# Performance work log

Measured on AMD Instinct MI355X. Metric: run time of the kernel, lower is better.

Reference implementation:

```python
import jax, jax.numpy as jnp
import numpy as np

B, L, C, S, W, R = 2, 16, 64, 64, 128, 32
MOD_HIDDEN = 32


def _conv3d(x, k, b, pad_hw):
    # x: (B,C,L,S,W), k: (O,I,1,kh,kw)
    y = jax.lax.conv_general_dilated(
        x, k, window_strides=(1, 1, 1),
        padding=((0, 0), (pad_hw, pad_hw), (pad_hw, pad_hw)),
        dimension_numbers=('NCDHW', 'OIDHW', 'NCDHW'))
    return y + b[None, :, None, None, None]


def setup_inputs() -> dict:
    key = jax.random.key(0)
    ks = jax.random.split(key, 16)
    d = {}
    d['x'] = jax.random.normal(ks[0], (B, L, C, S, W), jnp.float32)
    u1 = jax.random.uniform(ks[1], (C, R), jnp.float32)
    u2 = jax.random.uniform(ks[2], (C, R), jnp.float32)
    r_min, r_max = 0.8, 0.99
    d['nu_log'] = jnp.log(-0.5 * jnp.log(u1 * (r_max ** 2 - r_min ** 2) + r_min ** 2))
    d['theta_log'] = jnp.log(u2 * jnp.float32(2 * np.pi))
    d['disp_nu'] = jnp.zeros((C, R), jnp.float32)
    d['disp_theta'] = jnp.zeros((C, R), jnp.float32)
    d['mlp_w1'] = jax.random.normal(ks[3], (C, MOD_HIDDEN), jnp.float32) / np.sqrt(C).astype(np.float32)
    d['mlp_b1'] = jnp.zeros((MOD_HIDDEN,), jnp.float32)
    d['mlp_w2'] = jax.random.normal(ks[4], (MOD_HIDDEN, C * R * 2), jnp.float32) / np.sqrt(MOD_HIDDEN).astype(np.float32)
    d['mlp_b2'] = jnp.zeros((C * R * 2,), jnp.float32)
    d['forcing_scale'] = jnp.float32(0.1)
    d['U_row_r'] = jax.random.normal(ks[5], (C, S, R), jnp.float32) / np.sqrt(S).astype(np.float32)
    d['U_row_i'] = jax.random.normal(ks[6], (C, S, R), jnp.float32) / np.sqrt(S).astype(np.float32)
    d['V_col_r'] = jax.random.normal(ks[7], (C, W, R), jnp.float32) / np.sqrt(W).astype(np.float32)
    d['V_col_i'] = jax.random.normal(ks[8], (C, W, R), jnp.float32) / np.sqrt(W).astype(np.float32)
    d['proj_W_r'] = jax.random.normal(ks[9], (C, C), jnp.float32) / np.sqrt(C).astype(np.float32)
    d['proj_W_i'] = jax.random.normal(ks[10], (C, C), jnp.float32) / np.sqrt(C).astype(np.float32)
    d['proj_b_r'] = jnp.zeros((C,), jnp.float32)
    d['proj_b_i'] = jnp.zeros((C,), jnp.float32)
    fan = np.sqrt(C * 9).astype(np.float32)
    d['convr_k'] = jax.random.normal(ks[11], (C, C, 1, 3, 3), jnp.float32) / fan
    d['convr_b'] = jnp.zeros((C,), jnp.float32)
    d['convi_k'] = jax.random.normal(ks[12], (C, C, 1, 3, 3), jnp.float32) / fan
    d['convi_b'] = jnp.zeros((C,), jnp.float32)
    d['fuse_k'] = jax.random.normal(ks[13], (C, 2 * C, 1, 1, 1), jnp.float32) / np.sqrt(2 * C).astype(np.float32)
    d['fuse_b'] = jnp.zeros((C,), jnp.float32)
    d['ln_g'] = jnp.ones((S, W), jnp.float32)
    d['ln_b'] = jnp.zeros((S, W), jnp.float32)
    return d


def reference(x, nu_log, theta_log, disp_nu, disp_theta, mlp_w1, mlp_b1,
              mlp_w2, mlp_b2, forcing_scale, U_row_r, U_row_i, V_col_r,
              V_col_i, proj_W_r, proj_W_i, proj_b_r, proj_b_i, convr_k,
              convr_b, convi_k, convi_b, fuse_k, fuse_b, ln_g, ln_b):
    # Diagonal LRU poles lam = exp(-exp(nu) + i*exp(theta)), per (C,R)
    nu = jnp.exp(nu_log + disp_nu)
    theta = jnp.exp(theta_log + disp_theta)
    lam = jnp.exp(jax.lax.complex(-nu, theta))
    gamma = jnp.sqrt(jnp.clip(1.0 - jnp.abs(lam) ** 2, 1e-6, None))

    # Selective input-dependent forcing from spatially-pooled context
    ctx = x.mean(axis=(-2, -1))  # (B,L,C)
    f = jnp.tanh(ctx @ mlp_w1 + mlp_b1) @ mlp_w2 + mlp_b2
    f = f.reshape(ctx.shape[0], ctx.shape[1], C, R, 2)
    forcing = forcing_scale * jax.lax.complex(f[..., 0], f[..., 1])  # (B,L,C,R)

    # Low-rank complex spatial projection to rank-R state per channel
    U = jax.lax.complex(U_row_r, U_row_i)  # (C,S,R)
    V = jax.lax.complex(V_col_r, V_col_i)  # (C,W,R)
    xc = x.astype(jnp.complex64)
    u = jnp.einsum('blcsw,csr->blcwr', xc, jnp.conj(U))
    u = jnp.einsum('blcwr,cwr->blcr', u, jnp.conj(V))  # (B,L,C,R)
    u = gamma * u * (1.0 + forcing)

    # Diagonal linear recurrence h_t = lam*h_{t-1} + u_t via associative scan over L
    A = jnp.broadcast_to(lam[None, None], u.shape)

    def comb(e1, e2):
        a1, b1 = e1
        a2, b2 = e2
        return a1 * a2, a2 * b1 + b2

    _, h = jax.lax.associative_scan(comb, (A, u), axis=1)

    # Reconstruct spatial field from low-rank states
    t = jnp.einsum('blcr,csr->blcsr', h, U)
    y = jnp.einsum('blcsr,cwr->blcsw', t, V)  # (B,L,C,S,W) complex

    projW = jax.lax.complex(proj_W_r, proj_W_i)
    projb = jax.lax.complex(proj_b_r, proj_b_i)
    y = jnp.einsum('blcsw,oc->blosw', y, projW) + projb[None, None, :, None, None]

    # Post-recurrence spatial convs on real/imag parts, fuse, layernorm, residual
    yr = jnp.transpose(jnp.real(y), (0, 2, 1, 3, 4))  # (B,C,L,S,W)
    yi = jnp.transpose(jnp.imag(y), (0, 2, 1, 3, 4))
    yr = _conv3d(yr, convr_k, convr_b, 1)
    yi = _conv3d(yi, convi_k, convi_b, 1)
    fused = _conv3d(jnp.concatenate([yr, yi], axis=1), fuse_k, fuse_b, 0)
    fused = jnp.transpose(fused, (0, 2, 1, 3, 4))  # (B,L,C,S,W)

    mu = fused.mean(axis=(-2, -1), keepdims=True)
    var = fused.var(axis=(-2, -1), keepdims=True)
    normed = (fused - mu) / jnp.sqrt(var + 1e-5) * ln_g + ln_b
    return normed + x
```

## Files before the change

kernel.cpp:

```cpp
#include <hip/hip_runtime.h>

typedef unsigned short u16;
typedef unsigned int u32;
typedef __attribute__((ext_vector_type(8))) short short8;
typedef __attribute__((ext_vector_type(4))) float f32x4;

constexpr int B = 2, L = 16, C = 64, S = 64, W = 128, R = 32, MH = 32;
constexpr int BL = B * L;
constexpr int SW = S * W;
constexpr int CR = C * R;
constexpr int F2 = C * R * 2;

__device__ __forceinline__ float us2f(u16 h) { return __uint_as_float(((u32)h) << 16); }
__device__ __forceinline__ float bf_lo(u32 u) { return __uint_as_float(u << 16); }
__device__ __forceinline__ float bf_hi(u32 u) { return __uint_as_float(u & 0xffff0000u); }
__device__ __forceinline__ u16 f2bu(float f) {
  u32 u = __float_as_uint(f);
  u32 r = (u + 0x7fffu + ((u >> 16) & 1u)) >> 16;
  return (u16)r;
}
__device__ __forceinline__ u32 pack2(float lo, float hi) {
  return (u32)f2bu(lo) | ((u32)f2bu(hi) << 16);
}

__global__ void k_prep(const float* __restrict__ nu_log, const float* __restrict__ th_log,
                       const float* __restrict__ dnu, const float* __restrict__ dth,
                       float* __restrict__ lamr, float* __restrict__ lami,
                       float* __restrict__ gam) {
  int i = blockIdx.x * 256 + threadIdx.x;
  if (i >= CR) return;
  float nu = expf(nu_log[i] + dnu[i]);
  float th = expf(th_log[i] + dth[i]);
  float mag = expf(-nu);
  lamr[i] = mag * cosf(th);
  lami[i] = mag * sinf(th);
  gam[i] = sqrtf(fmaxf(1.0f - mag * mag, 1e-6f));
}

__global__ void k_keff(const float* __restrict__ fuse_k, const float* __restrict__ fuse_b,
                       const float* __restrict__ convr_k, const float* __restrict__ convr_b,
                       const float* __restrict__ convi_k, const float* __restrict__ convi_b,
                       u16* __restrict__ keff_bf, float* __restrict__ biaseff) {
  int i = blockIdx.x * 256 + threadIdx.x;
  if (i < C * 2 * C * 9) {
    int o = i / (2 * C * 9);
    int rem = i - o * (2 * C * 9);
    int cin2 = rem / 9;
    int seg = rem - cin2 * 9;
    const float* ck = (cin2 < C) ? convr_k : convi_k;
    int cin = cin2 & (C - 1);
    int fbase = o * 2 * C + ((cin2 < C) ? 0 : C);
    float acc = 0.f;
    for (int m = 0; m < C; ++m)
      acc += fuse_k[fbase + m] * ck[(m * C + cin) * 9 + seg];
    int kstep = cin2 >> 5;
    int kk = cin2 & 31;
    int lane = (o & 15) | ((kk >> 3) << 4);
    int j = kk & 7;
    int m_tile = o >> 4;
    keff_bf[((((seg * 4 + kstep) * 4 + m_tile) * 64 + lane) << 3) + j] = f2bu(acc);
  } else if (i < C * 2 * C * 9 + C) {
    int o = i - C * 2 * C * 9;
    float acc = fuse_b[o];
    for (int m = 0; m < C; ++m) {
      acc += fuse_k[o * 2 * C + m] * convr_b[m];
      acc += fuse_k[o * 2 * C + C + m] * convi_b[m];
    }
    biaseff[o] = acc;
  }
}

__global__ void k_apack(const float* __restrict__ pWr, const float* __restrict__ pWi,
                        u16* __restrict__ aproj) {
  int i = blockIdx.x * 256 + threadIdx.x;
  if (i >= 128 * 128) return;
  int m = i >> 7, k = i & 127;
  int c = k >> 1, im = k & 1;
  int o = m & 63;
  float v;
  if (m < 64) v = im ? -pWi[o * 64 + c] : pWr[o * 64 + c];
  else        v = im ?  pWr[o * 64 + c] : pWi[o * 64 + c];
  aproj[i] = f2bu(v);
}

__global__ __launch_bounds__(256) void k_mlp(
    const float* __restrict__ ctx, const float* __restrict__ w1, const float* __restrict__ b1,
    const float* __restrict__ w2, const float* __restrict__ b2, const float* __restrict__ fscale,
    float* __restrict__ forcing) {
  int bl = blockIdx.x >> 4;
  int kt = blockIdx.x & 15;
  int k0 = kt * 256;
  __shared__ float cv[C];
  __shared__ float hid[MH];
  __shared__ float lw2[MH * 256];
  int t = threadIdx.x;
  if (t < C) cv[t] = ctx[bl * C + t];
  for (int i = t; i < MH * 64; i += 256) {
    int j = i >> 6, q = i & 63;
    ((float4*)lw2)[i] = ((const float4*)(w2 + (size_t)j * F2 + k0))[q];
  }
  __syncthreads();
  if (t < MH) {
    float a = b1[t];
    for (int c2 = 0; c2 < C; ++c2) a += cv[c2] * w1[c2 * MH + t];
    hid[t] = tanhf(a);
  }
  __syncthreads();
  float scale = fscale[0];
  float a = b2[k0 + t];
#pragma unroll
  for (int j = 0; j < MH; ++j) a += hid[j] * lw2[j * 256 + t];
  forcing[(size_t)bl * F2 + k0 + t] = scale * a;
}

__global__ __launch_bounds__(256) void k_enc(
    const float* __restrict__ x,
    const float* __restrict__ Vr, const float* __restrict__ Vi,
    const float* __restrict__ Ur, const float* __restrict__ Ui,
    float* __restrict__ ctx, float* __restrict__ u) {
  int blc = blockIdx.x;
  int c = blc & (C - 1);
  __shared__ __align__(16) char smem[17408 * 2 + 16384 + 64];
  u16* xt = (u16*)smem;
  u16* bt = (u16*)(smem + 17408);
  float* uldr = (float*)(smem + 34816);
  float* uldi = uldr + 2048;
  float* y1  = (float*)smem;
  float* part = (float*)(smem + 17408);
  float* red = (float*)(smem + 17408 * 2 + 16384);
  int t = threadIdx.x;
  int lane = t & 63, wv = t >> 6;
  float sm = 0.f;
  {
    const float4* xp = (const float4*)(x + (size_t)blc * SW);
    for (int i = t; i < SW / 4; i += 256) {
      float4 v = xp[i];
      sm += v.x + v.y + v.z + v.w;
      int idx = i * 4, s = idx >> 7, w = idx & 127;
      u32* d = (u32*)&xt[s * 136 + w];
      d[0] = pack2(v.x, v.y);
      d[1] = pack2(v.z, v.w);
    }
  }
#pragma unroll
  for (int o = 32; o > 0; o >>= 1) sm += __shfl_down(sm, o, 64);
  if (lane == 0) red[wv] = sm;
  {
    const float* vrp = Vr + (size_t)c * 4096;
    const float* vip = Vi + (size_t)c * 4096;
    for (int i = t; i < 4096; i += 256) {
      int w = i >> 5, r = i & 31;
      bt[r * 136 + w]        = f2bu(vrp[i]);
      bt[(32 + r) * 136 + w] = f2bu(-vip[i]);
    }
  }
  {
    const float* urp = Ur + (size_t)c * 2048;
    const float* uip = Ui + (size_t)c * 2048;
    for (int i = t; i < 2048; i += 256) { uldr[i] = urp[i]; uldi[i] = uip[i]; }
  }
  __syncthreads();
  if (t == 0) ctx[blc] = (red[0] + red[1] + red[2] + red[3]) * (1.f / SW);
  int quad = lane >> 4, l15 = lane & 15;
  f32x4 zf = {0.f, 0.f, 0.f, 0.f};
  f32x4 acc[4] = {zf, zf, zf, zf};
#pragma unroll
  for (int ks = 0; ks < 4; ++ks) {
    int kofs = ks * 32 + quad * 8;
    short8 bf = *(const short8*)&bt[(wv * 16 + l15) * 136 + kofs];
#pragma unroll
    for (int mt = 0; mt < 4; ++mt) {
      short8 af = *(const short8*)&xt[(mt * 16 + l15) * 136 + kofs];
      acc[mt] = __builtin_amdgcn_mfma_f32_16x16x32_bf16(af, bf, acc[mt], 0, 0, 0);
    }
  }
  __syncthreads();
#pragma unroll
  for (int mt = 0; mt < 4; ++mt)
#pragma unroll
    for (int reg = 0; reg < 4; ++reg)
      y1[(mt * 16 + quad * 4 + reg) * 65 + wv * 16 + l15] = acc[mt][reg];
  __syncthreads();
  {
    int r = t & 31, sg = t >> 5;
    float pr = 0.f, pi = 0.f;
#pragma unroll
    for (int k = 0; k < 8; ++k) {
      int s = sg * 8 + k;
      float yr = y1[s * 65 + r], yi = y1[s * 65 + 32 + r];
      float ur = uldr[s * 32 + r], ui = uldi[s * 32 + r];
      pr += ur * yr + ui * yi;
      pi += ur * yi - ui * yr;
    }
    part[sg * 64 + r * 2]     = pr;
    part[sg * 64 + r * 2 + 1] = pi;
  }
  __syncthreads();
  if (t < 32) {
    float pr = 0.f, pi = 0.f;
#pragma unroll
    for (int sg = 0; sg < 8; ++sg) {
      pr += part[sg * 64 + t * 2];
      pi += part[sg * 64 + t * 2 + 1];
    }
    u[((size_t)blc * R + t) * 2]     = pr;
    u[((size_t)blc * R + t) * 2 + 1] = pi;
  }
}

__global__ void k_scan(const float* __restrict__ lamr, const float* __restrict__ lami,
                       const float* __restrict__ gam, const float* __restrict__ forcing,
                       const float* __restrict__ u, float* __restrict__ h) {
  int i = blockIdx.x * 256 + threadIdx.x;
  if (i >= B * CR) return;
  int b = i / CR;
  int cr = i - b * CR;
  float lr = lamr[cr], li = lami[cr], g = gam[cr];
  float hr = 0.f, hi = 0.f;
  for (int l = 0; l < L; ++l) {
    size_t off = ((size_t)(b * L + l) * CR + cr) * 2;
    float ur0 = u[off], ui0 = u[off + 1];
    float fr = forcing[off], fi = forcing[off + 1];
    float ofr = 1.f + fr;
    float ur = g * (ur0 * ofr - ui0 * fi);
    float ui = g * (ur0 * fi + ui0 * ofr);
    float nr = lr * hr - li * hi + ur;
    float ni = lr * hi + li * hr + ui;
    hr = nr; hi = ni;
    h[off] = hr; h[off + 1] = hi;
  }
}

__global__ __launch_bounds__(256) void k_decode(
    const float* __restrict__ h,
    const float* __restrict__ Ur, const float* __restrict__ Ui,
    const float* __restrict__ Vr, const float* __restrict__ Vi,
    u32* __restrict__ y_cm32, int bl_base) {
  int bid = blockIdx.x;
  int c = bid & 63;
  int blh = bid >> 6;
  int bl = bl_base + blh;
  __shared__ __align__(16) u16 ldA[64 * 72];
  __shared__ __align__(16) u16 ldBr[128 * 72];
  __shared__ __align__(16) u16 ldBi[128 * 72];
  int t = threadIdx.x;
  {
    const float* hp = h + ((size_t)(bl * C + c) * R) * 2;
    const float* urp = Ur + (size_t)c * (S * R);
    const float* uip = Ui + (size_t)c * (S * R);
    for (int p = t; p < S * R; p += 256) {
      int s = p >> 5, r = p & 31;
      float hr = hp[r * 2], hi = hp[r * 2 + 1];
      float ur = urp[p], ui = uip[p];
      ldA[s * 72 + r]      = f2bu(hr * ur - hi * ui);
      ldA[s * 72 + 32 + r] = f2bu(hr * ui + hi * ur);
    }
  }
  {
    const float* vrp = Vr + (size_t)c * (W * R);
    const float* vip = Vi + (size_t)c * (W * R);
    for (int p = t; p < W * R; p += 256) {
      int w = p >> 5, r = p & 31;
      float vr = vrp[p], vi = vip[p];
      ldBr[w * 72 + r]      = f2bu(vr);
      ldBr[w * 72 + 32 + r] = f2bu(-vi);
      ldBi[w * 72 + r]      = f2bu(vi);
      ldBi[w * 72 + 32 + r] = f2bu(vr);
    }
  }
  __syncthreads();
  int lane = t & 63, q = t >> 6;
  int quad = lane >> 4, l15 = lane & 15;
  f32x4 zf = {0.f, 0.f, 0.f, 0.f};
  f32x4 accr[4][2], acci[4][2];
#pragma unroll
  for (int mt = 0; mt < 4; ++mt)
#pragma unroll
    for (int nt = 0; nt < 2; ++nt) { accr[mt][nt] = zf; acci[mt][nt] = zf; }
#pragma unroll
  for (int ks = 0; ks < 2; ++ks) {
    int kofs = ks * 32 + quad * 8;
    short8 af[4];
#pragma unroll
    for (int mt = 0; mt < 4; ++mt)
      af[mt] = *(const short8*)&ldA[(mt * 16 + l15) * 72 + kofs];
#pragma unroll
    for (int nt = 0; nt < 2; ++nt) {
      int wrow = q * 32 + nt * 16 + l15;
      short8 br = *(const short8*)&ldBr[wrow * 72 + kofs];
      short8 bi = *(const short8*)&ldBi[wrow * 72 + kofs];
#pragma unroll
      for (int mt = 0; mt < 4; ++mt) {
        accr[mt][nt] = __builtin_amdgcn_mfma_f32_16x16x32_bf16(af[mt], br, accr[mt][nt], 0, 0, 0);
        acci[mt][nt] = __builtin_amdgcn_mfma_f32_16x16x32_bf16(af[mt], bi, acci[mt][nt], 0, 0, 0);
      }
    }
  }
  u32* dst = y_cm32 + ((size_t)(blh * 64 + c) << 13);
#pragma unroll
  for (int mt = 0; mt < 4; ++mt) {
#pragma unroll
    for (int nt = 0; nt < 2; ++nt) {
      int w = q * 32 + nt * 16 + l15;
#pragma unroll
      for (int reg = 0; reg < 4; ++reg) {
        int s = mt * 16 + quad * 4 + reg;
        dst[s * 128 + w] = pack2(accr[mt][nt][reg], acci[mt][nt][reg]);
      }
    }
  }
}

__global__ __launch_bounds__(256) void k_proj(
    const u32* __restrict__ y_cm32, const u16* __restrict__ aproj,
    const float* __restrict__ pbr, const float* __restrict__ pbi,
    u16* __restrict__ ynhwc, int bl_base) {
  int bid = blockIdx.x;
  int ntile = bid & 15;
  int blh = bid >> 4;
  int bl = bl_base + blh;
  __shared__ __align__(16) u16 lda[128 * 136];
  __shared__ __align__(16) u32 ldb[128 * 68];
  __shared__ float ldbias[128];
  int t = threadIdx.x;
  for (int i = t; i < 128 * 16; i += 256) {
    int m = i >> 4, qq = i & 15;
    ((uint4*)&lda[m * 136])[qq] = ((const uint4*)&aproj[m * 128])[qq];
  }
  if (t < 128) ldbias[t] = t < 64 ? pbr[t] : pbi[t - 64];

  int lane = t & 63, wv = t >> 6;
  int quad = lane >> 4, l15 = lane & 15;
  int cidx = t & 63, seg = t >> 6;
  f32x4 zf = {0.f, 0.f, 0.f, 0.f};

  for (int chunk = 0; chunk < 4; ++chunk) {
    int n0 = ntile * 512 + chunk * 128;
    __syncthreads();
    {
      const uint4* src = (const uint4*)(y_cm32 + (((size_t)(blh * 64 + cidx)) << 13) + n0 + seg * 32);
      u32 tmp[32];
#pragma unroll
      for (int qq = 0; qq < 8; ++qq) {
        uint4 v = src[qq];
        tmp[qq * 4] = v.x; tmp[qq * 4 + 1] = v.y; tmp[qq * 4 + 2] = v.z; tmp[qq * 4 + 3] = v.w;
      }
#pragma unroll
      for (int j = 0; j < 32; ++j)
        ldb[(seg * 32 + j) * 68 + cidx] = tmp[j];
    }
    __syncthreads();
    f32x4 acc[8][2];
#pragma unroll
    for (int mt = 0; mt < 8; ++mt) { acc[mt][0] = zf; acc[mt][1] = zf; }
    const u16* ldb16 = (const u16*)ldb;
#pragma unroll
    for (int ks = 0; ks < 4; ++ks) {
      int kofs = ks * 32 + quad * 8;
      short8 af[8];
#pragma unroll
      for (int mt = 0; mt < 8; ++mt)
        af[mt] = *(const short8*)&lda[(mt * 16 + l15) * 136 + kofs];
#pragma unroll
      for (int nt = 0; nt < 2; ++nt) {
        int nrow = wv * 32 + nt * 16 + l15;
        short8 bf = *(const short8*)&ldb16[nrow * 136 + kofs];
#pragma unroll
        for (int mt = 0; mt < 8; ++mt)
          acc[mt][nt] = __builtin_amdgcn_mfma_f32_16x16x32_bf16(af[mt], bf, acc[mt][nt], 0, 0, 0);
      }
    }
#pragma unroll
    for (int nt = 0; nt < 2; ++nt) {
      int n = n0 + wv * 32 + nt * 16 + l15;
      u16* drow = ynhwc + (((size_t)bl * SW + n) << 7);
#pragma unroll
      for (int mt = 0; mt < 8; ++mt) {
        int ch = mt * 16 + quad * 4;
        u32 lo = pack2(acc[mt][nt][0] + ldbias[ch],     acc[mt][nt][1] + ldbias[ch + 1]);
        u32 hi = pack2(acc[mt][nt][2] + ldbias[ch + 2], acc[mt][nt][3] + ldbias[ch + 3]);
        u32* dp = (u32*)(drow + ch);
        dp[0] = lo; dp[1] = hi;
      }
    }
  }
}

__global__ __launch_bounds__(256, 8) void k_conv(
    const u16* __restrict__ ynhwc, const u16* __restrict__ keff_bf,
    const float* __restrict__ biaseff, u16* __restrict__ fused) {
  int bid = blockIdx.x;
  int wt = bid & 3;
  int st = (bid >> 2) & 31;
  int bl = bid >> 7;
  int s0 = st * 2;
  int w0 = wt * 32;
  __shared__ __align__(16) u16 win[4][34][72];
  int t = threadIdx.x;
  int c_lo = (w0 == 0) ? 1 : 0;
  int c_hi = (w0 == 96) ? 33 : 34;
  uint4 z4 = make_uint4(0u, 0u, 0u, 0u);

  int lane = t & 63;
  int wv = t >> 6;
  int mp = wv & 1;
  int np = wv >> 1;
  int quad = lane >> 4, l15 = lane & 15;
  int chq = quad * 8;

  f32x4 zf = {0.f, 0.f, 0.f, 0.f};
  f32x4 acc[2][2];
  acc[0][0] = zf; acc[0][1] = zf; acc[1][0] = zf; acc[1][1] = zf;
  const short8* ap = (const short8*)keff_bf;

#pragma unroll
  for (int p = 0; p < 2; ++p) {
    if (p) __syncthreads();
    for (int rr = 0; rr < 4; ++rr) {
      int rs = s0 - 1 + rr;
      if (rs < 0 || rs >= S) {
        for (int i = t; i < 34 * 8; i += 256) {
          int col = i >> 3, q = i & 7;
          ((uint4*)&win[rr][col][0])[q] = z4;
        }
      } else {
        if (w0 == 0 && t < 8) ((uint4*)&win[rr][0][0])[t] = z4;
        if (w0 == 96 && t < 8) ((uint4*)&win[rr][33][0])[t] = z4;
        const uint4* src = (const uint4*)(ynhwc +
            (((size_t)bl * S + rs) * W + (w0 - 1 + c_lo)) * 128 + p * 64);
        int n4 = (c_hi - c_lo) * 8;
        for (int i = t; i < n4; i += 256) {
          int col = i >> 3, q = i & 7;
          ((uint4*)&win[rr][c_lo + col][0])[q] = src[col * 16 + q];
        }
      }
    }
    __syncthreads();

#pragma unroll
    for (int seg = 0; seg < 9; ++seg) {
      const int dr = seg / 3;
      const int dc = seg - dr * 3;
      const u16* b0base = &win[np + dr][l15 + dc][0];
      const u16* b1base = b0base + 16 * 72;
#pragma unroll
      for (int ks2 = 0; ks2 < 2; ++ks2) {
        const int ks = p * 2 + ks2;
        short8 a0 = ap[((seg * 4 + ks) * 4 + 2 * mp) * 64 + lane];
        short8 a1 = ap[((seg * 4 + ks) * 4 + 2 * mp + 1) * 64 + lane];
        short8 b0 = *(const short8*)(b0base + chq + ks2 * 32);
        short8 b1 = *(const short8*)(b1base + chq + ks2 * 32);
        acc[0][0] = __builtin_amdgcn_mfma_f32_16x16x32_bf16(a0, b0, acc[0][0], 0, 0, 0);
        acc[0][1] = __builtin_amdgcn_mfma_f32_16x16x32_bf16(a0, b1, acc[0][1], 0, 0, 0);
        acc[1][0] = __builtin_amdgcn_mfma_f32_16x16x32_bf16(a1, b0, acc[1][0], 0, 0, 0);
        acc[1][1] = __builtin_amdgcn_mfma_f32_16x16x32_bf16(a1, b1, acc[1][1], 0, 0, 0);
      }
    }
  }

  int s_out = s0 + np;
#pragma unroll
  for (int mi = 0; mi < 2; ++mi) {
#pragma unroll
    for (int reg = 0; reg < 4; ++reg) {
      int o = (2 * mp + mi) * 16 + quad * 4 + reg;
      float bias = biaseff[o];
      size_t rowoff = ((size_t)(bl * C + o) * S + s_out) * W;
      fused[rowoff + w0 + l15]      = f2bu(acc[mi][0][reg] + bias);
      fused[rowoff + w0 + 16 + l15] = f2bu(acc[mi][1][reg] + bias);
    }
  }
}

__global__ __launch_bounds__(256) void k_ln(
    const u16* __restrict__ fused,
    const float* __restrict__ ln_g, const float* __restrict__ ln_b,
    const float* __restrict__ x, float* __restrict__ out) {
  int blc = blockIdx.x;
  __shared__ u16 fs[SW];
  __shared__ float red[12];
  int t = threadIdx.x;
  const uint4* fp = (const uint4*)(fused + (size_t)blc * SW);
  float sm = 0.f, sq = 0.f;
  for (int i = t; i < SW / 8; i += 256) {
    uint4 v = fp[i];
    ((uint4*)fs)[i] = v;
    float f0 = bf_lo(v.x), f1 = bf_hi(v.x), f2 = bf_lo(v.y), f3 = bf_hi(v.y);
    float f4 = bf_lo(v.z), f5 = bf_hi(v.z), f6 = bf_lo(v.w), f7 = bf_hi(v.w);
    sm += f0 + f1 + f2 + f3 + f4 + f5 + f6 + f7;
    sq += f0 * f0 + f1 * f1 + f2 * f2 + f3 * f3 + f4 * f4 + f5 * f5 + f6 * f6 + f7 * f7;
  }
#pragma unroll
  for (int off = 32; off > 0; off >>= 1) {
    sm += __shfl_down(sm, off, 64);
    sq += __shfl_down(sq, off, 64);
  }
  int lane = t & 63, wid = t >> 6;
  if (lane == 0) { red[wid * 2] = sm; red[wid * 2 + 1] = sq; }
  __syncthreads();
  if (t == 0) {
    float S1 = red[0] + red[2] + red[4] + red[6];
    float S2 = red[1] + red[3] + red[5] + red[7];
    float mu = S1 * (1.f / SW);
    float var = S2 * (1.f / SW) - mu * mu;
    red[8] = mu;
    red[9] = rsqrtf(var + 1e-5f);
  }
  __syncthreads();
  float mu = red[8], rstd = red[9];
  const float* xp = x + (size_t)blc * SW;
  float* op = out + (size_t)blc * SW;
  for (int i = t; i < SW; i += 256)
    op[i] = (us2f(fs[i]) - mu) * rstd * ln_g[i] + ln_b[i] + xp[i];
}

extern "C" void kernel_launch(void* const* d_in, const int* in_sizes, int n_in,
                              void* d_out, int out_size, void* d_ws, size_t ws_size,
                              hipStream_t stream) {
  (void)in_sizes; (void)n_in; (void)out_size; (void)ws_size;
  const float* x       = (const float*)d_in[0];
  const float* nu_log  = (const float*)d_in[1];
  const float* th_log  = (const float*)d_in[2];
  const float* dnu     = (const float*)d_in[3];
  const float* dth     = (const float*)d_in[4];
  const float* w1      = (const float*)d_in[5];
  const float* b1      = (const float*)d_in[6];
  const float* w2      = (const float*)d_in[7];
  const float* b2      = (const float*)d_in[8];
  const float* fscale  = (const float*)d_in[9];
  const float* Ur      = (const float*)d_in[10];
  const float* Ui      = (const float*)d_in[11];
  const float* Vr      = (const float*)d_in[12];
  const float* Vi      = (const float*)d_in[13];
  const float* pWr     = (const float*)d_in[14];
  const float* pWi     = (const float*)d_in[15];
  const float* pbr     = (const float*)d_in[16];
  const float* pbi     = (const float*)d_in[17];
  const float* convr_k = (const float*)d_in[18];
  const float* convr_b = (const float*)d_in[19];
  const float* convi_k = (const float*)d_in[20];
  const float* convi_b = (const float*)d_in[21];
  const float* fuse_k  = (const float*)d_in[22];
  const float* fuse_b  = (const float*)d_in[23];
  const float* ln_g    = (const float*)d_in[24];
  const float* ln_b    = (const float*)d_in[25];
  float* out = (float*)d_out;

  char* ws = (char*)d_ws;
  float* lamr    = (float*)ws;
  float* lami    = lamr + 2048;
  float* gam     = lami + 2048;
  float* biaseff = gam + 2048;
  float* ctx     = biaseff + 64;
  float* forcing = ctx + 2048;
  float* ubuf    = forcing + 131072;
  float* hbuf    = ubuf + 131072;
  u16* keff_bf   = (u16*)(hbuf + 131072);
  u16* aproj     = keff_bf + 73728;
  size_t off = ((size_t)((char*)(aproj + 16384) - ws) + 255) & ~(size_t)255;
  u32* y_cm32    = (u32*)(ws + off);
  u16* fused     = (u16*)y_cm32;
  u16* ynhwc     = (u16*)(ws + off + (size_t)32 * 1024 * 1024);

  k_prep<<<8, 256, 0, stream>>>(nu_log, th_log, dnu, dth, lamr, lami, gam);
  k_keff<<<289, 256, 0, stream>>>(fuse_k, fuse_b, convr_k, convr_b, convi_k, convi_b,
                                  keff_bf, biaseff);
  k_apack<<<64, 256, 0, stream>>>(pWr, pWi, aproj);
  k_enc<<<BL * C, 256, 0, stream>>>(x, Vr, Vi, Ur, Ui, ctx, ubuf);
  k_mlp<<<BL * 16, 256, 0, stream>>>(ctx, w1, b1, w2, b2, fscale, forcing);
  k_scan<<<16, 256, 0, stream>>>(lamr, lami, gam, forcing, ubuf, hbuf);
  k_decode<<<1024, 256, 0, stream>>>(hbuf, Ur, Ui, Vr, Vi, y_cm32, 0);
  k_proj<<<256, 256, 0, stream>>>(y_cm32, aproj, pbr, pbi, ynhwc, 0);
  k_decode<<<1024, 256, 0, stream>>>(hbuf, Ur, Ui, Vr, Vi, y_cm32, 16);
  k_proj<<<256, 256, 0, stream>>>(y_cm32, aproj, pbr, pbi, ynhwc, 16);
  k_conv<<<4096, 256, 0, stream>>>(ynhwc, keff_bf, biaseff, fused);
  k_ln<<<BL * C, 256, 0, stream>>>(fused, ln_g, ln_b, x, out);
}
```

Baseline: 374.1 us.

## Widen conv tile to 64 columns and double-buffer weight fragment loads

The fused 3x3 conv kernel now processes 64 output columns per block instead of 32, halving the block count. Each A (weight) fragment is reused across four N tiles, and the halo overhead per block shrinks. Weight fragments for the next segment are prefetched into registers while the current segment's MFMAs run. The cost is more accumulator and buffer registers and more LDS per block (launch bounds lowered to 4 blocks), so occupancy drops.

```diff
diff --git a/kernel.cpp b/kernel.cpp
--- a/kernel.cpp
+++ b/kernel.cpp
@@ -386,19 +386,19 @@
   }
 }
 
-__global__ __launch_bounds__(256, 8) void k_conv(
+__global__ __launch_bounds__(256, 4) void k_conv(
     const u16* __restrict__ ynhwc, const u16* __restrict__ keff_bf,
     const float* __restrict__ biaseff, u16* __restrict__ fused) {
   int bid = blockIdx.x;
-  int wt = bid & 3;
-  int st = (bid >> 2) & 31;
-  int bl = bid >> 7;
+  int wt = bid & 1;
+  int st = (bid >> 1) & 31;
+  int bl = bid >> 6;
   int s0 = st * 2;
-  int w0 = wt * 32;
-  __shared__ __align__(16) u16 win[4][34][72];
+  int w0 = wt * 64;
+  __shared__ __align__(16) u16 win[4][66][72];
   int t = threadIdx.x;
-  int c_lo = (w0 == 0) ? 1 : 0;
-  int c_hi = (w0 == 96) ? 33 : 34;
+  int c_lo = (wt == 0) ? 1 : 0;
+  int c_hi = (wt == 0) ? 66 : 65;
   uint4 z4 = make_uint4(0u, 0u, 0u, 0u);
 
   int lane = t & 63;
@@ -409,9 +409,13 @@
   int chq = quad * 8;
 
   f32x4 zf = {0.f, 0.f, 0.f, 0.f};
-  f32x4 acc[2][2];
-  acc[0][0] = zf; acc[0][1] = zf; acc[1][0] = zf; acc[1][1] = zf;
+  f32x4 acc[2][4];
+#pragma unroll
+  for (int mi = 0; mi < 2; ++mi)
+#pragma unroll
+    for (int nt = 0; nt < 4; ++nt) acc[mi][nt] = zf;
   const short8* ap = (const short8*)keff_bf;
+  short8 abuf[2][2][2];
 
 #pragma unroll
   for (int p = 0; p < 2; ++p) {
@@ -419,13 +423,13 @@
     for (int rr = 0; rr < 4; ++rr) {
       int rs = s0 - 1 + rr;
       if (rs < 0 || rs >= S) {
-        for (int i = t; i < 34 * 8; i += 256) {
+        for (int i = t; i < 66 * 8; i += 256) {
           int col = i >> 3, q = i & 7;
           ((uint4*)&win[rr][col][0])[q] = z4;
         }
       } else {
-        if (w0 == 0 && t < 8) ((uint4*)&win[rr][0][0])[t] = z4;
-        if (w0 == 96 && t < 8) ((uint4*)&win[rr][33][0])[t] = z4;
+        if (wt == 0 && t < 8) ((uint4*)&win[rr][0][0])[t] = z4;
+        if (wt == 1 && t < 8) ((uint4*)&win[rr][65][0])[t] = z4;
         const uint4* src = (const uint4*)(ynhwc +
             (((size_t)bl * S + rs) * W + (w0 - 1 + c_lo)) * 128 + p * 64);
         int n4 = (c_hi - c_lo) * 8;
@@ -438,22 +442,35 @@
     __syncthreads();
 
 #pragma unroll
+    for (int ks2 = 0; ks2 < 2; ++ks2) {
+      const int ks = p * 2 + ks2;
+      abuf[0][0][ks2] = ap[((0 * 4 + ks) * 4 + 2 * mp) * 64 + lane];
+      abuf[0][1][ks2] = ap[((0 * 4 + ks) * 4 + 2 * mp + 1) * 64 + lane];
+    }
+
+#pragma unroll
     for (int seg = 0; seg < 9; ++seg) {
+      const int cur = seg & 1;
+      const int nxt = cur ^ 1;
+      if (seg < 8) {
+#pragma unroll
+        for (int ks2 = 0; ks2 < 2; ++ks2) {
+          const int ks = p * 2 + ks2;
+          abuf[nxt][0][ks2] = ap[(((seg + 1) * 4 + ks) * 4 + 2 * mp) * 64 + lane];
+          abuf[nxt][1][ks2] = ap[(((seg + 1) * 4 + ks) * 4 + 2 * mp + 1) * 64 + lane];
+        }
+      }
       const int dr = seg / 3;
       const int dc = seg - dr * 3;
-      const u16* b0base = &win[np + dr][l15 + dc][0];
-      const u16* b1base = b0base + 16 * 72;
+      const u16* rowbase = &win[np + dr][0][0];
 #pragma unroll
       for (int ks2 = 0; ks2 < 2; ++ks2) {
-        const int ks = p * 2 + ks2;
-        short8 a0 = ap[((seg * 4 + ks) * 4 + 2 * mp) * 64 + lane];
-        short8 a1 = ap[((seg * 4 + ks) * 4 + 2 * mp + 1) * 64 + lane];
-        short8 b0 = *(const short8*)(b0base + chq + ks2 * 32);
-        short8 b1 = *(const short8*)(b1base + chq + ks2 * 32);
-        acc[0][0] = __builtin_amdgcn_mfma_f32_16x16x32_bf16(a0, b0, acc[0][0], 0, 0, 0);
-        acc[0][1] = __builtin_amdgcn_mfma_f32_16x16x32_bf16(a0, b1, acc[0][1], 0, 0, 0);
-        acc[1][0] = __builtin_amdgcn_mfma_f32_16x16x32_bf16(a1, b0, acc[1][0], 0, 0, 0);
-        acc[1][1] = __builtin_amdgcn_mfma_f32_16x16x32_bf16(a1, b1, acc[1][1], 0, 0, 0);
+#pragma unroll
+        for (int nt = 0; nt < 4; ++nt) {
+          short8 b = *(const short8*)(rowbase + (nt * 16 + l15 + dc) * 72 + chq + ks2 * 32);
+          acc[0][nt] = __builtin_amdgcn_mfma_f32_16x16x32_bf16(abuf[cur][0][ks2], b, acc[0][nt], 0, 0, 0);
+          acc[1][nt] = __builtin_amdgcn_mfma_f32_16x16x32_bf16(abuf[cur][1][ks2], b, acc[1][nt], 0, 0, 0);
+        }
       }
     }
   }
@@ -466,8 +483,9 @@
       int o = (2 * mp + mi) * 16 + quad * 4 + reg;
       float bias = biaseff[o];
       size_t rowoff = ((size_t)(bl * C + o) * S + s_out) * W;
-      fused[rowoff + w0 + l15]      = f2bu(acc[mi][0][reg] + bias);
-      fused[rowoff + w0 + 16 + l15] = f2bu(acc[mi][1][reg] + bias);
+#pragma unroll
+      for (int nt = 0; nt < 4; ++nt)
+        fused[rowoff + w0 + nt * 16 + l15] = f2bu(acc[mi][nt][reg] + bias);
     }
   }
 }
@@ -573,6 +591,6 @@
   k_proj<<<256, 256, 0, stream>>>(y_cm32, aproj, pbr, pbi, ynhwc, 0);
   k_decode<<<1024, 256, 0, stream>>>(hbuf, Ur, Ui, Vr, Vi, y_cm32, 16);
   k_proj<<<256, 256, 0, stream>>>(y_cm32, aproj, pbr, pbi, ynhwc, 16);
-  k_conv<<<4096, 256, 0, stream>>>(ynhwc, keff_bf, biaseff, fused);
+  k_conv<<<2048, 256, 0, stream>>>(ynhwc, keff_bf, biaseff, fused);
   k_ln<<<BL * C, 256, 0, stream>>>(fused, ln_g, ln_b, x, out);
 }
```

Result: faster. 347.5 us (-7.1%).

## Enlarge conv tile to four output rows per block with double-buffered weight loads

Applied to the files above, without the earlier changes.

The fused 3x3 conv kernel now computes four output rows per block instead of two. Each wave handles one row and all 64 output channels, so the shared-memory halo overhead per output drops from 4/2 to 6/4 rows, and B fragments from LDS are reused across four M tiles. Weight fragments are software-prefetched from global memory into a two-slot register buffer. The cost is more accumulators and registers per thread (launch bounds lowered to 4 blocks), more LDS per block, and half as many blocks.

```diff
diff --git a/kernel.cpp b/kernel.cpp
--- a/kernel.cpp
+++ b/kernel.cpp
@@ -386,16 +386,16 @@
   }
 }
 
-__global__ __launch_bounds__(256, 8) void k_conv(
+__global__ __launch_bounds__(256, 4) void k_conv(
     const u16* __restrict__ ynhwc, const u16* __restrict__ keff_bf,
     const float* __restrict__ biaseff, u16* __restrict__ fused) {
   int bid = blockIdx.x;
   int wt = bid & 3;
-  int st = (bid >> 2) & 31;
-  int bl = bid >> 7;
-  int s0 = st * 2;
+  int st = (bid >> 2) & 15;
+  int bl = bid >> 6;
+  int s0 = st * 4;
   int w0 = wt * 32;
-  __shared__ __align__(16) u16 win[4][34][72];
+  __shared__ __align__(16) u16 win[6][34][72];
   int t = threadIdx.x;
   int c_lo = (w0 == 0) ? 1 : 0;
   int c_hi = (w0 == 96) ? 33 : 34;
@@ -403,20 +403,20 @@
 
   int lane = t & 63;
   int wv = t >> 6;
-  int mp = wv & 1;
-  int np = wv >> 1;
   int quad = lane >> 4, l15 = lane & 15;
   int chq = quad * 8;
 
   f32x4 zf = {0.f, 0.f, 0.f, 0.f};
-  f32x4 acc[2][2];
-  acc[0][0] = zf; acc[0][1] = zf; acc[1][0] = zf; acc[1][1] = zf;
+  f32x4 acc[4][2];
+#pragma unroll
+  for (int mt = 0; mt < 4; ++mt) { acc[mt][0] = zf; acc[mt][1] = zf; }
   const short8* ap = (const short8*)keff_bf;
+  short8 abuf[2][4];
 
 #pragma unroll
   for (int p = 0; p < 2; ++p) {
     if (p) __syncthreads();
-    for (int rr = 0; rr < 4; ++rr) {
+    for (int rr = 0; rr < 6; ++rr) {
       int rs = s0 - 1 + rr;
       if (rs < 0 || rs >= S) {
         for (int i = t; i < 34 * 8; i += 256) {
@@ -438,36 +438,46 @@
     __syncthreads();
 
 #pragma unroll
-    for (int seg = 0; seg < 9; ++seg) {
+    for (int mt = 0; mt < 4; ++mt)
+      abuf[0][mt] = ap[((0 * 4 + p * 2 + 0) * 4 + mt) * 64 + lane];
+
+#pragma unroll
+    for (int k = 0; k < 18; ++k) {
+      const int cur = k & 1;
+      const int nxt = cur ^ 1;
+      if (k < 17) {
+        const int k1 = k + 1;
+        const int seg1 = k1 >> 1, ks21 = k1 & 1;
+        const int ks1 = p * 2 + ks21;
+#pragma unroll
+        for (int mt = 0; mt < 4; ++mt)
+          abuf[nxt][mt] = ap[((seg1 * 4 + ks1) * 4 + mt) * 64 + lane];
+      }
+      const int seg = k >> 1;
+      const int ks2 = k & 1;
       const int dr = seg / 3;
       const int dc = seg - dr * 3;
-      const u16* b0base = &win[np + dr][l15 + dc][0];
-      const u16* b1base = b0base + 16 * 72;
-#pragma unroll
-      for (int ks2 = 0; ks2 < 2; ++ks2) {
-        const int ks = p * 2 + ks2;
-        short8 a0 = ap[((seg * 4 + ks) * 4 + 2 * mp) * 64 + lane];
-        short8 a1 = ap[((seg * 4 + ks) * 4 + 2 * mp + 1) * 64 + lane];
-        short8 b0 = *(const short8*)(b0base + chq + ks2 * 32);
-        short8 b1 = *(const short8*)(b1base + chq + ks2 * 32);
-        acc[0][0] = __builtin_amdgcn_mfma_f32_16x16x32_bf16(a0, b0, acc[0][0], 0, 0, 0);
-        acc[0][1] = __builtin_amdgcn_mfma_f32_16x16x32_bf16(a0, b1, acc[0][1], 0, 0, 0);
-        acc[1][0] = __builtin_amdgcn_mfma_f32_16x16x32_bf16(a1, b0, acc[1][0], 0, 0, 0);
-        acc[1][1] = __builtin_amdgcn_mfma_f32_16x16x32_bf16(a1, b1, acc[1][1], 0, 0, 0);
-      }
-    }
-  }
-
-  int s_out = s0 + np;
-#pragma unroll
-  for (int mi = 0; mi < 2; ++mi) {
+      const u16* bbase = &win[wv + dr][l15 + dc][chq + ks2 * 32];
+      short8 b0 = *(const short8*)bbase;
+      short8 b1 = *(const short8*)(bbase + 16 * 72);
+#pragma unroll
+      for (int mt = 0; mt < 4; ++mt) {
+        acc[mt][0] = __builtin_amdgcn_mfma_f32_16x16x32_bf16(abuf[cur][mt], b0, acc[mt][0], 0, 0, 0);
+        acc[mt][1] = __builtin_amdgcn_mfma_f32_16x16x32_bf16(abuf[cur][mt], b1, acc[mt][1], 0, 0, 0);
+      }
+    }
+  }
+
+  int s_out = s0 + wv;
+#pragma unroll
+  for (int mt = 0; mt < 4; ++mt) {
 #pragma unroll
     for (int reg = 0; reg < 4; ++reg) {
-      int o = (2 * mp + mi) * 16 + quad * 4 + reg;
+      int o = mt * 16 + quad * 4 + reg;
       float bias = biaseff[o];
       size_t rowoff = ((size_t)(bl * C + o) * S + s_out) * W;
-      fused[rowoff + w0 + l15]      = f2bu(acc[mi][0][reg] + bias);
-      fused[rowoff + w0 + 16 + l15] = f2bu(acc[mi][1][reg] + bias);
+      fused[rowoff + w0 + l15]      = f2bu(acc[mt][0][reg] + bias);
+      fused[rowoff + w0 + 16 + l15] = f2bu(acc[mt][1][reg] + bias);
     }
   }
 }
@@ -573,6 +583,6 @@
   k_proj<<<256, 256, 0, stream>>>(y_cm32, aproj, pbr, pbi, ynhwc, 0);
   k_decode<<<1024, 256, 0, stream>>>(hbuf, Ur, Ui, Vr, Vi, y_cm32, 16);
   k_proj<<<256, 256, 0, stream>>>(y_cm32, aproj, pbr, pbi, ynhwc, 16);
-  k_conv<<<4096, 256, 0, stream>>>(ynhwc, keff_bf, biaseff, fused);
+  k_conv<<<2048, 256, 0, stream>>>(ynhwc, keff_bf, biaseff, fused);
   k_ln<<<BL * C, 256, 0, stream>>>(fused, ln_g, ln_b, x, out);
 }
```

Result: faster. 365.4 us (-2.3%).
